# Kernel optimization log

Measured on AMD Instinct MI355X. Metric: run time of the kernel, lower is better.

Reference implementation:

```python
import jax, jax.numpy as jnp
import numpy as np

N, E, B = 200000, 6400000, 128
IN_LOCAL, IN_GLOBAL, HIDDEN, NUM_CLASSES = 16, 8, 32, 2


def setup_inputs() -> dict:
    key = jax.random.key(0)
    ks = jax.random.split(key, 16)
    inp = {
        "x_local": jax.random.normal(ks[0], (N, IN_LOCAL), dtype=jnp.float32),
        "x_global": jax.random.normal(ks[1], (B, IN_GLOBAL), dtype=jnp.float32),
        "batch": jnp.sort(jax.random.randint(ks[2], (N,), 0, B, dtype=jnp.int64)),
        "edge_index": jax.random.randint(ks[3], (2, E), 0, N, dtype=jnp.int64),
        # encoder params
        "W_local": jax.random.normal(ks[4], (IN_LOCAL, HIDDEN), jnp.float32) / np.sqrt(IN_LOCAL),
        "b_local": jnp.zeros((HIDDEN,), jnp.float32),
        "W_global": jax.random.normal(ks[5], (IN_GLOBAL, HIDDEN), jnp.float32) / np.sqrt(IN_GLOBAL),
        "b_global": jnp.zeros((HIDDEN,), jnp.float32),
        "W_mix": jax.random.normal(ks[6], (3 * HIDDEN, HIDDEN), jnp.float32) / np.sqrt(3 * HIDDEN),
        "b_mix": jnp.zeros((HIDDEN,), jnp.float32),
        # GNN layer params
        "W_msg": jax.random.normal(ks[7], (HIDDEN, HIDDEN), jnp.float32) / np.sqrt(HIDDEN),
        "b_msg": jnp.zeros((HIDDEN,), jnp.float32),
        "W_self": jax.random.normal(ks[8], (HIDDEN, HIDDEN), jnp.float32) / np.sqrt(HIDDEN),
        "b_self": jnp.zeros((HIDDEN,), jnp.float32),
        # output head
        "W_out": jax.random.normal(ks[9], (HIDDEN, NUM_CLASSES), jnp.float32) / np.sqrt(HIDDEN),
        "b_out": jnp.zeros((NUM_CLASSES,), jnp.float32),
    }
    return inp


def reference(x_local, x_global, batch, edge_index,
              W_local, b_local, W_global, b_global, W_mix, b_mix,
              W_msg, b_msg, W_self, b_self, W_out, b_out):
    n = x_local.shape[0]
    # --- MixedSelectivityNodeEncoder ---
    h_local = jax.nn.relu(x_local @ W_local + b_local)            # [N,H]
    h_global_graph = jax.nn.relu(x_global @ W_global + b_global)  # [B,H]
    h_global = h_global_graph[batch]                              # gather -> [N,H]
    h_int = h_local * h_global
    h_cat = jnp.concatenate([h_local, h_global, h_int], axis=-1)  # [N,3H]
    h0 = jax.nn.relu(h_cat @ W_mix + b_mix)                       # [N,H]
    # --- GNN layer with self loops, add aggregation ---
    loops = jnp.arange(n, dtype=edge_index.dtype)
    src = jnp.concatenate([edge_index[0], loops])                 # [E+N]
    dst = jnp.concatenate([edge_index[1], loops])                 # [E+N]
    msg = jax.nn.relu(h0[src] @ W_msg + b_msg)                    # [E+N,H]
    aggr = jax.ops.segment_sum(msg, dst, num_segments=n)          # [N,H]
    h = jax.nn.relu(aggr + h0 @ W_self + b_self)                  # [N,H]
    # --- output head ---
    return h @ W_out + b_out                                      # [N,C]
```

## Files before the change

kernel.cpp:

```cpp
#include <hip/hip_runtime.h>

#define N_NODES  200000
#define N_EDGES  6400000
#define NGRAPH   128
#define H        32

#define BNODES   256
#define NBUCK    782
#define P_BLOCKS 256
#define EPB      25000
#define SORT_CAP 8960


typedef unsigned short ushort_t;

__device__ __forceinline__ ushort_t f32_to_bf16_rne(float f) {
    unsigned u = __float_as_uint(f);
    unsigned r = (u + 0x7fffu + ((u >> 16) & 1u)) >> 16;
    return (ushort_t)r;
}
__device__ __forceinline__ float bf16_to_f32(ushort_t h) {
    return __uint_as_float(((unsigned)h) << 16);
}

__global__ __launch_bounds__(256, 1) void k_node_enc(
        const float* __restrict__ xl,
        const int*   __restrict__ batch,
        const float* __restrict__ xg,   const float* __restrict__ Wg,
        const float* __restrict__ bg,
        const float* __restrict__ Wl,   const float* __restrict__ bl,
        const float* __restrict__ Wmix, const float* __restrict__ bmix,
        const float* __restrict__ Wmsg, const float* __restrict__ bmsg,
        const float* __restrict__ Wself,const float* __restrict__ bself,
        ushort_t* __restrict__ mb, float* __restrict__ s) {
    int n0 = blockIdx.x * 256 + threadIdx.x;
    bool valid = (n0 < N_NODES);
    int n = valid ? n0 : (N_NODES - 1);

    float xv[16];
    {
        const float4* p = (const float4*)(xl + (size_t)n * 16);
        float4 a = p[0], b = p[1], c = p[2], d = p[3];
        xv[0]=a.x; xv[1]=a.y; xv[2]=a.z; xv[3]=a.w;
        xv[4]=b.x; xv[5]=b.y; xv[6]=b.z; xv[7]=b.w;
        xv[8]=c.x; xv[9]=c.y; xv[10]=c.z; xv[11]=c.w;
        xv[12]=d.x; xv[13]=d.y; xv[14]=d.z; xv[15]=d.w;
    }
    float gvv[8];
    {
        int gb = batch[n];
        const float4* q = (const float4*)(xg + (size_t)gb * 8);
        float4 a = q[0], b = q[1];
        gvv[0]=a.x; gvv[1]=a.y; gvv[2]=a.z; gvv[3]=a.w;
        gvv[4]=b.x; gvv[5]=b.y; gvv[6]=b.z; gvv[7]=b.w;
    }

    float hl[32], hg[32], hi[32];
#pragma unroll
    for (int t4 = 0; t4 < 8; ++t4) {
        float4 al = ((const float4*)bl)[t4];
        float4 ag = ((const float4*)bg)[t4];
#pragma unroll
        for (int k = 0; k < 16; ++k) {
            float4 w = ((const float4*)(Wl + k * H))[t4];
            al.x = fmaf(xv[k], w.x, al.x); al.y = fmaf(xv[k], w.y, al.y);
            al.z = fmaf(xv[k], w.z, al.z); al.w = fmaf(xv[k], w.w, al.w);
        }
#pragma unroll
        for (int k = 0; k < 8; ++k) {
            float4 w = ((const float4*)(Wg + k * H))[t4];
            ag.x = fmaf(gvv[k], w.x, ag.x); ag.y = fmaf(gvv[k], w.y, ag.y);
            ag.z = fmaf(gvv[k], w.z, ag.z); ag.w = fmaf(gvv[k], w.w, ag.w);
        }
        hl[t4*4+0] = fmaxf(al.x, 0.f); hl[t4*4+1] = fmaxf(al.y, 0.f);
        hl[t4*4+2] = fmaxf(al.z, 0.f); hl[t4*4+3] = fmaxf(al.w, 0.f);
        hg[t4*4+0] = fmaxf(ag.x, 0.f); hg[t4*4+1] = fmaxf(ag.y, 0.f);
        hg[t4*4+2] = fmaxf(ag.z, 0.f); hg[t4*4+3] = fmaxf(ag.w, 0.f);
    }
#pragma unroll
    for (int k = 0; k < 32; ++k) hi[k] = hl[k] * hg[k];

    float h0[32];
#pragma unroll
    for (int t4 = 0; t4 < 8; ++t4) {
        float4 acc = ((const float4*)bmix)[t4];
#pragma unroll
        for (int k = 0; k < 32; ++k) {
            float4 w = ((const float4*)(Wmix + k * H))[t4];
            acc.x = fmaf(hl[k], w.x, acc.x); acc.y = fmaf(hl[k], w.y, acc.y);
            acc.z = fmaf(hl[k], w.z, acc.z); acc.w = fmaf(hl[k], w.w, acc.w);
        }
#pragma unroll
        for (int k = 0; k < 32; ++k) {
            float4 w = ((const float4*)(Wmix + (32 + k) * H))[t4];
            acc.x = fmaf(hg[k], w.x, acc.x); acc.y = fmaf(hg[k], w.y, acc.y);
            acc.z = fmaf(hg[k], w.z, acc.z); acc.w = fmaf(hg[k], w.w, acc.w);
        }
#pragma unroll
        for (int k = 0; k < 32; ++k) {
            float4 w = ((const float4*)(Wmix + (64 + k) * H))[t4];
            acc.x = fmaf(hi[k], w.x, acc.x); acc.y = fmaf(hi[k], w.y, acc.y);
            acc.z = fmaf(hi[k], w.z, acc.z); acc.w = fmaf(hi[k], w.w, acc.w);
        }
        h0[t4*4+0] = fmaxf(acc.x, 0.f); h0[t4*4+1] = fmaxf(acc.y, 0.f);
        h0[t4*4+2] = fmaxf(acc.z, 0.f); h0[t4*4+3] = fmaxf(acc.w, 0.f);
    }

#pragma unroll
    for (int t4 = 0; t4 < 8; ++t4) {
        float4 am = ((const float4*)bmsg)[t4];
        float4 as = ((const float4*)bself)[t4];
#pragma unroll
        for (int k = 0; k < 32; ++k) {
            float4 wm = ((const float4*)(Wmsg + k * H))[t4];
            float4 ws = ((const float4*)(Wself + k * H))[t4];
            am.x = fmaf(h0[k], wm.x, am.x); am.y = fmaf(h0[k], wm.y, am.y);
            am.z = fmaf(h0[k], wm.z, am.z); am.w = fmaf(h0[k], wm.w, am.w);
            as.x = fmaf(h0[k], ws.x, as.x); as.y = fmaf(h0[k], ws.y, as.y);
            as.z = fmaf(h0[k], ws.z, as.z); as.w = fmaf(h0[k], ws.w, as.w);
        }
        if (valid) {
            unsigned d0 = (unsigned)f32_to_bf16_rne(fmaxf(am.x, 0.f))
                        | ((unsigned)f32_to_bf16_rne(fmaxf(am.y, 0.f)) << 16);
            unsigned d1 = (unsigned)f32_to_bf16_rne(fmaxf(am.z, 0.f))
                        | ((unsigned)f32_to_bf16_rne(fmaxf(am.w, 0.f)) << 16);
            ((unsigned*)(mb + (size_t)n * H))[t4*2+0] = d0;
            ((unsigned*)(mb + (size_t)n * H))[t4*2+1] = d1;
            ((float4*)(s + (size_t)n * H))[t4] = as;
        }
    }
}

__global__ __launch_bounds__(1024) void k_ppart(
        const int* __restrict__ ei,
        int* __restrict__ gcur,
        unsigned int* __restrict__ ebuf) {
    __shared__ int cnt[NBUCK];
    __shared__ int basex[NBUCK];
    int t = threadIdx.x, blk = blockIdx.x;
    for (int i = t; i < NBUCK; i += 1024) cnt[i] = 0;
    __syncthreads();

    int e0 = blk * EPB, e1 = e0 + EPB;
    for (int e = e0 + t; e < e1; e += 1024)
        atomicAdd(&cnt[ei[N_EDGES + e] >> 8], 1);
    __syncthreads();

    for (int i = t; i < NBUCK; i += 1024) {
        int c = cnt[i];
        basex[i] = (c > 0) ? atomicAdd(&gcur[i * 32], c) : 0;
    }
    __syncthreads();

    for (int e = e0 + t; e < e1; e += 1024) {
        unsigned src = (unsigned)ei[e];
        int dst = ei[N_EDGES + e];
        int bkt = dst >> 8;
        int pos = atomicAdd(&basex[bkt], 1);
        if (pos < SORT_CAP)
            ebuf[(size_t)bkt * SORT_CAP + pos] = (src << 8) | (unsigned)(dst & 255);
    }
}

__global__ __launch_bounds__(512, 8) void k_bsort_aggr(
        const int* __restrict__ gcur,
        const unsigned int* __restrict__ ebuf,
        const ushort_t* __restrict__ mb, const float* __restrict__ s,
        const float* __restrict__ Wout, const float* __restrict__ bout,
        float* __restrict__ out) {
    __shared__ unsigned sorted[SORT_CAP];
    __shared__ int cnt[BNODES];
    __shared__ int offx[BNODES + 1];
    __shared__ int cur[BNODES];
    __shared__ int wsum[4];
    int tid = threadIdx.x, b = blockIdx.x;

    size_t base = (size_t)b * SORT_CAP;
    int sz = min(gcur[b * 32], SORT_CAP);

    if (tid < BNODES) cnt[tid] = 0;
    __syncthreads();

    for (int j = tid; j < sz; j += 512)
        atomicAdd(&cnt[ebuf[base + j] & 255], 1);
    __syncthreads();

    {
        int lane = tid & 63, w = tid >> 6;
        int v = (tid < BNODES) ? cnt[tid] : 0;
#pragma unroll
        for (int d = 1; d < 64; d <<= 1) {
            int u = __shfl_up(v, d, 64);
            if (lane >= d) v += u;
        }
        if (tid < BNODES && lane == 63) wsum[w] = v;
        __syncthreads();
        if (tid < BNODES) {
            int add = 0;
#pragma unroll
            for (int i = 0; i < 3; ++i) add += (i < w) ? wsum[i] : 0;
            int inc = v + add;
            offx[tid + 1] = inc;
            cur[tid] = inc - cnt[tid];
            if (tid == 0) offx[0] = 0;
        }
        __syncthreads();
    }

    for (int j = tid; j < sz; j += 512) {
        unsigned pk = ebuf[base + j];
        int pos = atomicAdd(&cur[pk & 255], 1);
        sorted[pos] = pk;
    }
    __syncthreads();

    const unsigned* mb32 = (const unsigned*)mb;
    int g = tid >> 4;
    int t = tid & 15;

    for (int q = 0; q < 8; ++q) {
        int loc = (g << 3) + q;
        int n = b * BNODES + loc;
        int rs = offx[loc];
        int re = offx[loc + 1];
        float a0 = 0.f, a1 = 0.f;

        for (int j = rs; j < re; j += 8) {
            unsigned pk[8], u[8];
#pragma unroll
            for (int k = 0; k < 8; ++k)
                pk[k] = sorted[min(j + k, re - 1)];
#pragma unroll
            for (int k = 0; k < 8; ++k)
                u[k] = mb32[(pk[k] >> 8) * 16u + (unsigned)t];
#pragma unroll
            for (int k = 0; k < 8; ++k) {
                bool ok = (j + k < re);
                a0 += ok ? __uint_as_float(u[k] << 16)         : 0.f;
                a1 += ok ? __uint_as_float(u[k] & 0xffff0000u) : 0.f;
            }
        }

        if (n < N_NODES) {
            unsigned u = mb32[(unsigned)n * 16u + (unsigned)t];
            float2 sv = *(const float2*)(s + (size_t)n * H + 2 * t);
            float h0 = fmaxf(a0 + __uint_as_float(u << 16)         + sv.x, 0.f);
            float h1 = fmaxf(a1 + __uint_as_float(u & 0xffff0000u) + sv.y, 0.f);
            float4 w = *(const float4*)(Wout + 4 * t);
            float p0 = h0 * w.x + h1 * w.z;
            float p1 = h0 * w.y + h1 * w.w;
#pragma unroll
            for (int o = 8; o >= 1; o >>= 1) {
                p0 += __shfl_down(p0, o, 16);
                p1 += __shfl_down(p1, o, 16);
            }
            if (t == 0) {
                float2 o2;
                o2.x = p0 + bout[0];
                o2.y = p1 + bout[1];
                *(float2*)(out + (size_t)n * 2) = o2;
            }
        }
    }
}

extern "C" void kernel_launch(void* const* d_in, const int* in_sizes, int n_in,
                              void* d_out, int out_size, void* d_ws, size_t ws_size,
                              hipStream_t stream) {
    const float* xl    = (const float*)d_in[0];
    const float* xg    = (const float*)d_in[1];
    const int*   batch = (const int*)  d_in[2];
    const int*   ei    = (const int*)  d_in[3];
    const float* Wl    = (const float*)d_in[4];
    const float* bl    = (const float*)d_in[5];
    const float* Wg    = (const float*)d_in[6];
    const float* bg    = (const float*)d_in[7];
    const float* Wmix  = (const float*)d_in[8];
    const float* bmix  = (const float*)d_in[9];
    const float* Wmsg  = (const float*)d_in[10];
    const float* bmsg  = (const float*)d_in[11];
    const float* Wself = (const float*)d_in[12];
    const float* bself = (const float*)d_in[13];
    const float* Wout  = (const float*)d_in[14];
    const float* bout  = (const float*)d_in[15];
    float* out = (float*)d_out;

    float*    s    = (float*)d_ws;
    ushort_t* mb   = (ushort_t*)(s + (size_t)N_NODES * H);
    int*      gcur = (int*)(mb + (size_t)N_NODES * H);
    unsigned int* ebuf = (unsigned int*)(gcur + (size_t)NBUCK * 32);

    k_node_enc<<<(N_NODES + 255) / 256, 256, 0, stream>>>(xl, batch, xg, Wg, bg,
                                                          Wl, bl, Wmix, bmix,
                                                          Wmsg, bmsg, Wself, bself,
                                                          mb, s);

    hipMemsetAsync(gcur, 0, (size_t)NBUCK * 32 * sizeof(int), stream);
    k_ppart<<<P_BLOCKS, 1024, 0, stream>>>(ei, gcur, ebuf);
    k_bsort_aggr<<<NBUCK, 512, 0, stream>>>(gcur, ebuf, mb, s, Wout, bout, out);
}
```

Baseline: 367.2 us.

## Merge node encoder and edge partition into one kernel, restructure encoder loops

Fuses the node-encoder kernel and the edge bucket-partition kernel into a single launch, with block index deciding the role, so the compute-bound encoder and the memory-bound partition can run concurrently. The encoder is also reworked to produce h_local/h_global one element at a time and accumulate into the mix output, and the msg and self projections are split into separate loops, all to cut register pressure. The partition blocks now use 256 threads instead of 1024, which lowers per-block parallelism in that phase.

Result: slower. 436.8 us (+18.9%).

```diff
diff --git a/kernel.cpp b/kernel.cpp
--- a/kernel.cpp
+++ b/kernel.cpp
@@ -9,6 +9,7 @@
 #define NBUCK    782
 #define P_BLOCKS 256
 #define EPB      25000
+#define ENC_BLOCKS 782
 #define SORT_CAP 8960
 
 
@@ -23,7 +24,7 @@
     return __uint_as_float(((unsigned)h) << 16);
 }
 
-__global__ __launch_bounds__(256, 1) void k_node_enc(
+__global__ __launch_bounds__(256, 1) void k_enc_part(
         const float* __restrict__ xl,
         const int*   __restrict__ batch,
         const float* __restrict__ xg,   const float* __restrict__ Wg,
@@ -32,8 +33,42 @@
         const float* __restrict__ Wmix, const float* __restrict__ bmix,
         const float* __restrict__ Wmsg, const float* __restrict__ bmsg,
         const float* __restrict__ Wself,const float* __restrict__ bself,
-        ushort_t* __restrict__ mb, float* __restrict__ s) {
-    int n0 = blockIdx.x * 256 + threadIdx.x;
+        ushort_t* __restrict__ mb, float* __restrict__ s,
+        const int* __restrict__ ei,
+        int* __restrict__ gcur,
+        unsigned int* __restrict__ ebuf) {
+    __shared__ int cnt[NBUCK];
+    __shared__ int basex[NBUCK];
+    int tid = threadIdx.x;
+
+    if (blockIdx.x >= ENC_BLOCKS) {
+        int blk = blockIdx.x - ENC_BLOCKS;
+        for (int i = tid; i < NBUCK; i += 256) cnt[i] = 0;
+        __syncthreads();
+
+        int e0 = blk * EPB, e1 = e0 + EPB;
+        for (int e = e0 + tid; e < e1; e += 256)
+            atomicAdd(&cnt[ei[N_EDGES + e] >> 8], 1);
+        __syncthreads();
+
+        for (int i = tid; i < NBUCK; i += 256) {
+            int c = cnt[i];
+            basex[i] = (c > 0) ? atomicAdd(&gcur[i * 32], c) : 0;
+        }
+        __syncthreads();
+
+        for (int e = e0 + tid; e < e1; e += 256) {
+            unsigned src = (unsigned)ei[e];
+            int dst = ei[N_EDGES + e];
+            int bkt = dst >> 8;
+            int pos = atomicAdd(&basex[bkt], 1);
+            if (pos < SORT_CAP)
+                ebuf[(size_t)bkt * SORT_CAP + pos] = (src << 8) | (unsigned)(dst & 255);
+        }
+        return;
+    }
+
+    int n0 = blockIdx.x * 256 + tid;
     bool valid = (n0 < N_NODES);
     int n = valid ? n0 : (N_NODES - 1);
 
@@ -55,69 +90,50 @@
         gvv[4]=b.x; gvv[5]=b.y; gvv[6]=b.z; gvv[7]=b.w;
     }
 
-    float hl[32], hg[32], hi[32];
+    float4 acc4[8];
+#pragma unroll
+    for (int t4 = 0; t4 < 8; ++t4) acc4[t4] = ((const float4*)bmix)[t4];
+
+#pragma unroll
+    for (int k = 0; k < 32; ++k) {
+        float hlk = bl[k];
+#pragma unroll
+        for (int j = 0; j < 16; ++j)
+            hlk = fmaf(xv[j], Wl[j * H + k], hlk);
+        hlk = fmaxf(hlk, 0.f);
+        float hgk = bg[k];
+#pragma unroll
+        for (int j = 0; j < 8; ++j)
+            hgk = fmaf(gvv[j], Wg[j * H + k], hgk);
+        hgk = fmaxf(hgk, 0.f);
+        float hik = hlk * hgk;
+#pragma unroll
+        for (int t4 = 0; t4 < 8; ++t4) {
+            float4 w1 = ((const float4*)(Wmix + k * H))[t4];
+            float4 w2 = ((const float4*)(Wmix + (32 + k) * H))[t4];
+            float4 w3 = ((const float4*)(Wmix + (64 + k) * H))[t4];
+            acc4[t4].x = fmaf(hlk, w1.x, fmaf(hgk, w2.x, fmaf(hik, w3.x, acc4[t4].x)));
+            acc4[t4].y = fmaf(hlk, w1.y, fmaf(hgk, w2.y, fmaf(hik, w3.y, acc4[t4].y)));
+            acc4[t4].z = fmaf(hlk, w1.z, fmaf(hgk, w2.z, fmaf(hik, w3.z, acc4[t4].z)));
+            acc4[t4].w = fmaf(hlk, w1.w, fmaf(hgk, w2.w, fmaf(hik, w3.w, acc4[t4].w)));
+        }
+    }
+
+    float h0[32];
 #pragma unroll
     for (int t4 = 0; t4 < 8; ++t4) {
-        float4 al = ((const float4*)bl)[t4];
-        float4 ag = ((const float4*)bg)[t4];
-#pragma unroll
-        for (int k = 0; k < 16; ++k) {
-            float4 w = ((const float4*)(Wl + k * H))[t4];
-            al.x = fmaf(xv[k], w.x, al.x); al.y = fmaf(xv[k], w.y, al.y);
-            al.z = fmaf(xv[k], w.z, al.z); al.w = fmaf(xv[k], w.w, al.w);
-        }
-#pragma unroll
-        for (int k = 0; k < 8; ++k) {
-            float4 w = ((const float4*)(Wg + k * H))[t4];
-            ag.x = fmaf(gvv[k], w.x, ag.x); ag.y = fmaf(gvv[k], w.y, ag.y);
-            ag.z = fmaf(gvv[k], w.z, ag.z); ag.w = fmaf(gvv[k], w.w, ag.w);
-        }
-        hl[t4*4+0] = fmaxf(al.x, 0.f); hl[t4*4+1] = fmaxf(al.y, 0.f);
-        hl[t4*4+2] = fmaxf(al.z, 0.f); hl[t4*4+3] = fmaxf(al.w, 0.f);
-        hg[t4*4+0] = fmaxf(ag.x, 0.f); hg[t4*4+1] = fmaxf(ag.y, 0.f);
-        hg[t4*4+2] = fmaxf(ag.z, 0.f); hg[t4*4+3] = fmaxf(ag.w, 0.f);
-    }
-#pragma unroll
-    for (int k = 0; k < 32; ++k) hi[k] = hl[k] * hg[k];
-
-    float h0[32];
-#pragma unroll
-    for (int t4 = 0; t4 < 8; ++t4) {
-        float4 acc = ((const float4*)bmix)[t4];
-#pragma unroll
-        for (int k = 0; k < 32; ++k) {
-            float4 w = ((const float4*)(Wmix + k * H))[t4];
-            acc.x = fmaf(hl[k], w.x, acc.x); acc.y = fmaf(hl[k], w.y, acc.y);
-            acc.z = fmaf(hl[k], w.z, acc.z); acc.w = fmaf(hl[k], w.w, acc.w);
-        }
-#pragma unroll
-        for (int k = 0; k < 32; ++k) {
-            float4 w = ((const float4*)(Wmix + (32 + k) * H))[t4];
-            acc.x = fmaf(hg[k], w.x, acc.x); acc.y = fmaf(hg[k], w.y, acc.y);
-            acc.z = fmaf(hg[k], w.z, acc.z); acc.w = fmaf(hg[k], w.w, acc.w);
-        }
-#pragma unroll
-        for (int k = 0; k < 32; ++k) {
-            float4 w = ((const float4*)(Wmix + (64 + k) * H))[t4];
-            acc.x = fmaf(hi[k], w.x, acc.x); acc.y = fmaf(hi[k], w.y, acc.y);
-            acc.z = fmaf(hi[k], w.z, acc.z); acc.w = fmaf(hi[k], w.w, acc.w);
-        }
-        h0[t4*4+0] = fmaxf(acc.x, 0.f); h0[t4*4+1] = fmaxf(acc.y, 0.f);
-        h0[t4*4+2] = fmaxf(acc.z, 0.f); h0[t4*4+3] = fmaxf(acc.w, 0.f);
+        h0[t4*4+0] = fmaxf(acc4[t4].x, 0.f); h0[t4*4+1] = fmaxf(acc4[t4].y, 0.f);
+        h0[t4*4+2] = fmaxf(acc4[t4].z, 0.f); h0[t4*4+3] = fmaxf(acc4[t4].w, 0.f);
     }
 
 #pragma unroll
     for (int t4 = 0; t4 < 8; ++t4) {
         float4 am = ((const float4*)bmsg)[t4];
-        float4 as = ((const float4*)bself)[t4];
 #pragma unroll
         for (int k = 0; k < 32; ++k) {
             float4 wm = ((const float4*)(Wmsg + k * H))[t4];
-            float4 ws = ((const float4*)(Wself + k * H))[t4];
             am.x = fmaf(h0[k], wm.x, am.x); am.y = fmaf(h0[k], wm.y, am.y);
             am.z = fmaf(h0[k], wm.z, am.z); am.w = fmaf(h0[k], wm.w, am.w);
-            as.x = fmaf(h0[k], ws.x, as.x); as.y = fmaf(h0[k], ws.y, as.y);
-            as.z = fmaf(h0[k], ws.z, as.z); as.w = fmaf(h0[k], ws.w, as.w);
         }
         if (valid) {
             unsigned d0 = (unsigned)f32_to_bf16_rne(fmaxf(am.x, 0.f))
@@ -126,39 +142,20 @@
                         | ((unsigned)f32_to_bf16_rne(fmaxf(am.w, 0.f)) << 16);
             ((unsigned*)(mb + (size_t)n * H))[t4*2+0] = d0;
             ((unsigned*)(mb + (size_t)n * H))[t4*2+1] = d1;
+        }
+    }
+
+#pragma unroll
+    for (int t4 = 0; t4 < 8; ++t4) {
+        float4 as = ((const float4*)bself)[t4];
+#pragma unroll
+        for (int k = 0; k < 32; ++k) {
+            float4 ws = ((const float4*)(Wself + k * H))[t4];
+            as.x = fmaf(h0[k], ws.x, as.x); as.y = fmaf(h0[k], ws.y, as.y);
+            as.z = fmaf(h0[k], ws.z, as.z); as.w = fmaf(h0[k], ws.w, as.w);
+        }
+        if (valid)
             ((float4*)(s + (size_t)n * H))[t4] = as;
-        }
-    }
-}
-
-__global__ __launch_bounds__(1024) void k_ppart(
-        const int* __restrict__ ei,
-        int* __restrict__ gcur,
-        unsigned int* __restrict__ ebuf) {
-    __shared__ int cnt[NBUCK];
-    __shared__ int basex[NBUCK];
-    int t = threadIdx.x, blk = blockIdx.x;
-    for (int i = t; i < NBUCK; i += 1024) cnt[i] = 0;
-    __syncthreads();
-
-    int e0 = blk * EPB, e1 = e0 + EPB;
-    for (int e = e0 + t; e < e1; e += 1024)
-        atomicAdd(&cnt[ei[N_EDGES + e] >> 8], 1);
-    __syncthreads();
-
-    for (int i = t; i < NBUCK; i += 1024) {
-        int c = cnt[i];
-        basex[i] = (c > 0) ? atomicAdd(&gcur[i * 32], c) : 0;
-    }
-    __syncthreads();
-
-    for (int e = e0 + t; e < e1; e += 1024) {
-        unsigned src = (unsigned)ei[e];
-        int dst = ei[N_EDGES + e];
-        int bkt = dst >> 8;
-        int pos = atomicAdd(&basex[bkt], 1);
-        if (pos < SORT_CAP)
-            ebuf[(size_t)bkt * SORT_CAP + pos] = (src << 8) | (unsigned)(dst & 255);
     }
 }
 
@@ -290,12 +287,12 @@
     int*      gcur = (int*)(mb + (size_t)N_NODES * H);
     unsigned int* ebuf = (unsigned int*)(gcur + (size_t)NBUCK * 32);
 
-    k_node_enc<<<(N_NODES + 255) / 256, 256, 0, stream>>>(xl, batch, xg, Wg, bg,
-                                                          Wl, bl, Wmix, bmix,
-                                                          Wmsg, bmsg, Wself, bself,
-                                                          mb, s);
-
     hipMemsetAsync(gcur, 0, (size_t)NBUCK * 32 * sizeof(int), stream);
-    k_ppart<<<P_BLOCKS, 1024, 0, stream>>>(ei, gcur, ebuf);
+
+    k_enc_part<<<ENC_BLOCKS + P_BLOCKS, 256, 0, stream>>>(
+        xl, batch, xg, Wg, bg, Wl, bl, Wmix, bmix,
+        Wmsg, bmsg, Wself, bself, mb, s,
+        ei, gcur, ebuf);
+
     k_bsort_aggr<<<NBUCK, 512, 0, stream>>>(gcur, ebuf, mb, s, Wout, bout, out);
 }
```

## Split node encoder across four lanes per node with wave shuffles

Applied to the files above, without the earlier changes.

The node encoder now assigns four threads to each node, with each thread computing eight of the 32 hidden channels. Intermediate activations are exchanged between the four lanes with wave shuffles. This cuts per-thread register pressure, which the old one-node-per-thread version with 96-float arrays had at occupancy 1, and raises parallelism to 3125 blocks. It costs extra shuffle instructions and redundant weight loads per lane. The memset is also moved ahead of the encoder launch.

Result: slower. 456.0 us (+24.2%).

```diff
diff --git a/kernel.cpp b/kernel.cpp
--- a/kernel.cpp
+++ b/kernel.cpp
@@ -19,11 +19,14 @@
     unsigned r = (u + 0x7fffu + ((u >> 16) & 1u)) >> 16;
     return (ushort_t)r;
 }
+__device__ __forceinline__ unsigned pack_bf16x2(float lo, float hi) {
+    return (unsigned)f32_to_bf16_rne(lo) | ((unsigned)f32_to_bf16_rne(hi) << 16);
+}
 __device__ __forceinline__ float bf16_to_f32(ushort_t h) {
     return __uint_as_float(((unsigned)h) << 16);
 }
 
-__global__ __launch_bounds__(256, 1) void k_node_enc(
+__global__ __launch_bounds__(256) void k_enc4(
         const float* __restrict__ xl,
         const int*   __restrict__ batch,
         const float* __restrict__ xg,   const float* __restrict__ Wg,
@@ -33,19 +36,15 @@
         const float* __restrict__ Wmsg, const float* __restrict__ bmsg,
         const float* __restrict__ Wself,const float* __restrict__ bself,
         ushort_t* __restrict__ mb, float* __restrict__ s) {
-    int n0 = blockIdx.x * 256 + threadIdx.x;
-    bool valid = (n0 < N_NODES);
-    int n = valid ? n0 : (N_NODES - 1);
-
-    float xv[16];
-    {
-        const float4* p = (const float4*)(xl + (size_t)n * 16);
-        float4 a = p[0], b = p[1], c = p[2], d = p[3];
-        xv[0]=a.x; xv[1]=a.y; xv[2]=a.z; xv[3]=a.w;
-        xv[4]=b.x; xv[5]=b.y; xv[6]=b.z; xv[7]=b.w;
-        xv[8]=c.x; xv[9]=c.y; xv[10]=c.z; xv[11]=c.w;
-        xv[12]=d.x; xv[13]=d.y; xv[14]=d.z; xv[15]=d.w;
-    }
+    int tid   = threadIdx.x;
+    int r     = tid & 3;
+    int n     = blockIdx.x * 64 + (tid >> 2);
+    int lane  = tid & 63;
+    int gbase = lane & 60;
+    int ch0   = 8 * r;
+
+    float4 xq = ((const float4*)(xl + (size_t)n * 16))[r];
+
     float gvv[8];
     {
         int gb = batch[n];
@@ -55,80 +54,118 @@
         gvv[4]=b.x; gvv[5]=b.y; gvv[6]=b.z; gvv[7]=b.w;
     }
 
-    float hl[32], hg[32], hi[32];
-#pragma unroll
-    for (int t4 = 0; t4 < 8; ++t4) {
-        float4 al = ((const float4*)bl)[t4];
-        float4 ag = ((const float4*)bg)[t4];
-#pragma unroll
-        for (int k = 0; k < 16; ++k) {
-            float4 w = ((const float4*)(Wl + k * H))[t4];
-            al.x = fmaf(xv[k], w.x, al.x); al.y = fmaf(xv[k], w.y, al.y);
-            al.z = fmaf(xv[k], w.z, al.z); al.w = fmaf(xv[k], w.w, al.w);
-        }
-#pragma unroll
-        for (int k = 0; k < 8; ++k) {
-            float4 w = ((const float4*)(Wg + k * H))[t4];
-            ag.x = fmaf(gvv[k], w.x, ag.x); ag.y = fmaf(gvv[k], w.y, ag.y);
-            ag.z = fmaf(gvv[k], w.z, ag.z); ag.w = fmaf(gvv[k], w.w, ag.w);
-        }
-        hl[t4*4+0] = fmaxf(al.x, 0.f); hl[t4*4+1] = fmaxf(al.y, 0.f);
-        hl[t4*4+2] = fmaxf(al.z, 0.f); hl[t4*4+3] = fmaxf(al.w, 0.f);
-        hg[t4*4+0] = fmaxf(ag.x, 0.f); hg[t4*4+1] = fmaxf(ag.y, 0.f);
-        hg[t4*4+2] = fmaxf(ag.z, 0.f); hg[t4*4+3] = fmaxf(ag.w, 0.f);
-    }
-#pragma unroll
-    for (int k = 0; k < 32; ++k) hi[k] = hl[k] * hg[k];
-
-    float h0[32];
-#pragma unroll
-    for (int t4 = 0; t4 < 8; ++t4) {
-        float4 acc = ((const float4*)bmix)[t4];
-#pragma unroll
-        for (int k = 0; k < 32; ++k) {
-            float4 w = ((const float4*)(Wmix + k * H))[t4];
-            acc.x = fmaf(hl[k], w.x, acc.x); acc.y = fmaf(hl[k], w.y, acc.y);
-            acc.z = fmaf(hl[k], w.z, acc.z); acc.w = fmaf(hl[k], w.w, acc.w);
-        }
-#pragma unroll
-        for (int k = 0; k < 32; ++k) {
-            float4 w = ((const float4*)(Wmix + (32 + k) * H))[t4];
-            acc.x = fmaf(hg[k], w.x, acc.x); acc.y = fmaf(hg[k], w.y, acc.y);
-            acc.z = fmaf(hg[k], w.z, acc.z); acc.w = fmaf(hg[k], w.w, acc.w);
-        }
-#pragma unroll
-        for (int k = 0; k < 32; ++k) {
-            float4 w = ((const float4*)(Wmix + (64 + k) * H))[t4];
-            acc.x = fmaf(hi[k], w.x, acc.x); acc.y = fmaf(hi[k], w.y, acc.y);
-            acc.z = fmaf(hi[k], w.z, acc.z); acc.w = fmaf(hi[k], w.w, acc.w);
-        }
-        h0[t4*4+0] = fmaxf(acc.x, 0.f); h0[t4*4+1] = fmaxf(acc.y, 0.f);
-        h0[t4*4+2] = fmaxf(acc.z, 0.f); h0[t4*4+3] = fmaxf(acc.w, 0.f);
-    }
-
-#pragma unroll
-    for (int t4 = 0; t4 < 8; ++t4) {
-        float4 am = ((const float4*)bmsg)[t4];
-        float4 as = ((const float4*)bself)[t4];
-#pragma unroll
-        for (int k = 0; k < 32; ++k) {
-            float4 wm = ((const float4*)(Wmsg + k * H))[t4];
-            float4 ws = ((const float4*)(Wself + k * H))[t4];
-            am.x = fmaf(h0[k], wm.x, am.x); am.y = fmaf(h0[k], wm.y, am.y);
-            am.z = fmaf(h0[k], wm.z, am.z); am.w = fmaf(h0[k], wm.w, am.w);
-            as.x = fmaf(h0[k], ws.x, as.x); as.y = fmaf(h0[k], ws.y, as.y);
-            as.z = fmaf(h0[k], ws.z, as.z); as.w = fmaf(h0[k], ws.w, as.w);
-        }
-        if (valid) {
-            unsigned d0 = (unsigned)f32_to_bf16_rne(fmaxf(am.x, 0.f))
-                        | ((unsigned)f32_to_bf16_rne(fmaxf(am.y, 0.f)) << 16);
-            unsigned d1 = (unsigned)f32_to_bf16_rne(fmaxf(am.z, 0.f))
-                        | ((unsigned)f32_to_bf16_rne(fmaxf(am.w, 0.f)) << 16);
-            ((unsigned*)(mb + (size_t)n * H))[t4*2+0] = d0;
-            ((unsigned*)(mb + (size_t)n * H))[t4*2+1] = d1;
-            ((float4*)(s + (size_t)n * H))[t4] = as;
-        }
-    }
+    float hlr[8];
+    {
+        float4 b0 = *(const float4*)(bl + ch0);
+        float4 b1 = *(const float4*)(bl + ch0 + 4);
+        hlr[0]=b0.x; hlr[1]=b0.y; hlr[2]=b0.z; hlr[3]=b0.w;
+        hlr[4]=b1.x; hlr[5]=b1.y; hlr[6]=b1.z; hlr[7]=b1.w;
+#pragma unroll
+        for (int j = 0; j < 16; ++j) {
+            float xvj = __shfl(((const float*)&xq)[j & 3], gbase | (j >> 2), 64);
+            float4 w0 = *(const float4*)(Wl + j * H + ch0);
+            float4 w1 = *(const float4*)(Wl + j * H + ch0 + 4);
+            hlr[0] = fmaf(xvj, w0.x, hlr[0]); hlr[1] = fmaf(xvj, w0.y, hlr[1]);
+            hlr[2] = fmaf(xvj, w0.z, hlr[2]); hlr[3] = fmaf(xvj, w0.w, hlr[3]);
+            hlr[4] = fmaf(xvj, w1.x, hlr[4]); hlr[5] = fmaf(xvj, w1.y, hlr[5]);
+            hlr[6] = fmaf(xvj, w1.z, hlr[6]); hlr[7] = fmaf(xvj, w1.w, hlr[7]);
+        }
+#pragma unroll
+        for (int i = 0; i < 8; ++i) hlr[i] = fmaxf(hlr[i], 0.f);
+    }
+
+    float hgr[8];
+    {
+        float4 b0 = *(const float4*)(bg + ch0);
+        float4 b1 = *(const float4*)(bg + ch0 + 4);
+        hgr[0]=b0.x; hgr[1]=b0.y; hgr[2]=b0.z; hgr[3]=b0.w;
+        hgr[4]=b1.x; hgr[5]=b1.y; hgr[6]=b1.z; hgr[7]=b1.w;
+#pragma unroll
+        for (int j = 0; j < 8; ++j) {
+            float gj = gvv[j];
+            float4 w0 = *(const float4*)(Wg + j * H + ch0);
+            float4 w1 = *(const float4*)(Wg + j * H + ch0 + 4);
+            hgr[0] = fmaf(gj, w0.x, hgr[0]); hgr[1] = fmaf(gj, w0.y, hgr[1]);
+            hgr[2] = fmaf(gj, w0.z, hgr[2]); hgr[3] = fmaf(gj, w0.w, hgr[3]);
+            hgr[4] = fmaf(gj, w1.x, hgr[4]); hgr[5] = fmaf(gj, w1.y, hgr[5]);
+            hgr[6] = fmaf(gj, w1.z, hgr[6]); hgr[7] = fmaf(gj, w1.w, hgr[7]);
+        }
+#pragma unroll
+        for (int i = 0; i < 8; ++i) hgr[i] = fmaxf(hgr[i], 0.f);
+    }
+
+    float acc[8];
+    {
+        float4 b0 = *(const float4*)(bmix + ch0);
+        float4 b1 = *(const float4*)(bmix + ch0 + 4);
+        acc[0]=b0.x; acc[1]=b0.y; acc[2]=b0.z; acc[3]=b0.w;
+        acc[4]=b1.x; acc[5]=b1.y; acc[6]=b1.z; acc[7]=b1.w;
+    }
+#pragma unroll
+    for (int k = 0; k < 32; ++k) {
+        int owner = gbase | (k >> 3);
+        float hlk = __shfl(hlr[k & 7], owner, 64);
+        float hgk = __shfl(hgr[k & 7], owner, 64);
+        float hik = hlk * hgk;
+        float4 w1a = *(const float4*)(Wmix + k * H + ch0);
+        float4 w1b = *(const float4*)(Wmix + k * H + ch0 + 4);
+        float4 w2a = *(const float4*)(Wmix + (32 + k) * H + ch0);
+        float4 w2b = *(const float4*)(Wmix + (32 + k) * H + ch0 + 4);
+        float4 w3a = *(const float4*)(Wmix + (64 + k) * H + ch0);
+        float4 w3b = *(const float4*)(Wmix + (64 + k) * H + ch0 + 4);
+        acc[0] = fmaf(hlk, w1a.x, fmaf(hgk, w2a.x, fmaf(hik, w3a.x, acc[0])));
+        acc[1] = fmaf(hlk, w1a.y, fmaf(hgk, w2a.y, fmaf(hik, w3a.y, acc[1])));
+        acc[2] = fmaf(hlk, w1a.z, fmaf(hgk, w2a.z, fmaf(hik, w3a.z, acc[2])));
+        acc[3] = fmaf(hlk, w1a.w, fmaf(hgk, w2a.w, fmaf(hik, w3a.w, acc[3])));
+        acc[4] = fmaf(hlk, w1b.x, fmaf(hgk, w2b.x, fmaf(hik, w3b.x, acc[4])));
+        acc[5] = fmaf(hlk, w1b.y, fmaf(hgk, w2b.y, fmaf(hik, w3b.y, acc[5])));
+        acc[6] = fmaf(hlk, w1b.z, fmaf(hgk, w2b.z, fmaf(hik, w3b.z, acc[6])));
+        acc[7] = fmaf(hlk, w1b.w, fmaf(hgk, w2b.w, fmaf(hik, w3b.w, acc[7])));
+    }
+    float h0r[8];
+#pragma unroll
+    for (int i = 0; i < 8; ++i) h0r[i] = fmaxf(acc[i], 0.f);
+
+    float am[8], as[8];
+    {
+        float4 m0 = *(const float4*)(bmsg + ch0);
+        float4 m1 = *(const float4*)(bmsg + ch0 + 4);
+        am[0]=m0.x; am[1]=m0.y; am[2]=m0.z; am[3]=m0.w;
+        am[4]=m1.x; am[5]=m1.y; am[6]=m1.z; am[7]=m1.w;
+        float4 s0 = *(const float4*)(bself + ch0);
+        float4 s1 = *(const float4*)(bself + ch0 + 4);
+        as[0]=s0.x; as[1]=s0.y; as[2]=s0.z; as[3]=s0.w;
+        as[4]=s1.x; as[5]=s1.y; as[6]=s1.z; as[7]=s1.w;
+    }
+#pragma unroll
+    for (int k = 0; k < 32; ++k) {
+        float h0k = __shfl(h0r[k & 7], gbase | (k >> 3), 64);
+        float4 wma = *(const float4*)(Wmsg + k * H + ch0);
+        float4 wmb = *(const float4*)(Wmsg + k * H + ch0 + 4);
+        float4 wsa = *(const float4*)(Wself + k * H + ch0);
+        float4 wsb = *(const float4*)(Wself + k * H + ch0 + 4);
+        am[0] = fmaf(h0k, wma.x, am[0]); am[1] = fmaf(h0k, wma.y, am[1]);
+        am[2] = fmaf(h0k, wma.z, am[2]); am[3] = fmaf(h0k, wma.w, am[3]);
+        am[4] = fmaf(h0k, wmb.x, am[4]); am[5] = fmaf(h0k, wmb.y, am[5]);
+        am[6] = fmaf(h0k, wmb.z, am[6]); am[7] = fmaf(h0k, wmb.w, am[7]);
+        as[0] = fmaf(h0k, wsa.x, as[0]); as[1] = fmaf(h0k, wsa.y, as[1]);
+        as[2] = fmaf(h0k, wsa.z, as[2]); as[3] = fmaf(h0k, wsa.w, as[3]);
+        as[4] = fmaf(h0k, wsb.x, as[4]); as[5] = fmaf(h0k, wsb.y, as[5]);
+        as[6] = fmaf(h0k, wsb.z, as[6]); as[7] = fmaf(h0k, wsb.w, as[7]);
+    }
+
+    uint4 d;
+    d.x = pack_bf16x2(fmaxf(am[0], 0.f), fmaxf(am[1], 0.f));
+    d.y = pack_bf16x2(fmaxf(am[2], 0.f), fmaxf(am[3], 0.f));
+    d.z = pack_bf16x2(fmaxf(am[4], 0.f), fmaxf(am[5], 0.f));
+    d.w = pack_bf16x2(fmaxf(am[6], 0.f), fmaxf(am[7], 0.f));
+    ((uint4*)(mb + (size_t)n * H))[r] = d;
+
+    float4 sv0, sv1;
+    sv0.x = as[0]; sv0.y = as[1]; sv0.z = as[2]; sv0.w = as[3];
+    sv1.x = as[4]; sv1.y = as[5]; sv1.z = as[6]; sv1.w = as[7];
+    ((float4*)(s + (size_t)n * H))[2 * r]     = sv0;
+    ((float4*)(s + (size_t)n * H))[2 * r + 1] = sv1;
 }
 
 __global__ __launch_bounds__(1024) void k_ppart(
@@ -290,12 +327,12 @@
     int*      gcur = (int*)(mb + (size_t)N_NODES * H);
     unsigned int* ebuf = (unsigned int*)(gcur + (size_t)NBUCK * 32);
 
-    k_node_enc<<<(N_NODES + 255) / 256, 256, 0, stream>>>(xl, batch, xg, Wg, bg,
-                                                          Wl, bl, Wmix, bmix,
-                                                          Wmsg, bmsg, Wself, bself,
-                                                          mb, s);
-
     hipMemsetAsync(gcur, 0, (size_t)NBUCK * 32 * sizeof(int), stream);
+
+    k_enc4<<<N_NODES / 64, 256, 0, stream>>>(
+        xl, batch, xg, Wg, bg, Wl, bl, Wmix, bmix,
+        Wmsg, bmsg, Wself, bself, mb, s);
+
     k_ppart<<<P_BLOCKS, 1024, 0, stream>>>(ei, gcur, ebuf);
     k_bsort_aggr<<<NBUCK, 512, 0, stream>>>(gcur, ebuf, mb, s, Wout, bout, out);
 }
```

## Merge edge partition and node encoder into one heterogeneous kernel launch

Applied to the files above, without the earlier changes.

Fuses the edge bucketing kernel and the node encoder into a single launch. The first 256 blocks do the partition, the remaining 782 blocks do the node encoding, so the two independent phases can run concurrently on the GPU and one launch boundary is removed. The partition blocks now use 256 threads instead of 1024, so each block does more serial work and shared-memory atomic parallelism per block drops. The encoder's launch bound of one block per CU may also limit occupancy for the partition blocks.

Measured after the change: 391.8 us. +6.7%, slower.

```diff
diff --git a/kernel.cpp b/kernel.cpp
--- a/kernel.cpp
+++ b/kernel.cpp
@@ -9,6 +9,7 @@
 #define NBUCK    782
 #define P_BLOCKS 256
 #define EPB      25000
+#define ENC_BLOCKS 782
 #define SORT_CAP 8960
 
 
@@ -23,7 +24,10 @@
     return __uint_as_float(((unsigned)h) << 16);
 }
 
-__global__ __launch_bounds__(256, 1) void k_node_enc(
+__global__ __launch_bounds__(256, 1) void k_part_enc(
+        const int*   __restrict__ ei,
+        int*         __restrict__ gcur,
+        unsigned int* __restrict__ ebuf,
         const float* __restrict__ xl,
         const int*   __restrict__ batch,
         const float* __restrict__ xg,   const float* __restrict__ Wg,
@@ -33,7 +37,38 @@
         const float* __restrict__ Wmsg, const float* __restrict__ bmsg,
         const float* __restrict__ Wself,const float* __restrict__ bself,
         ushort_t* __restrict__ mb, float* __restrict__ s) {
-    int n0 = blockIdx.x * 256 + threadIdx.x;
+    __shared__ int cnt[NBUCK];
+    __shared__ int basex[NBUCK];
+    int tid = threadIdx.x;
+
+    if (blockIdx.x < P_BLOCKS) {
+        int blk = blockIdx.x;
+        for (int i = tid; i < NBUCK; i += 256) cnt[i] = 0;
+        __syncthreads();
+
+        int e0 = blk * EPB, e1 = e0 + EPB;
+        for (int e = e0 + tid; e < e1; e += 256)
+            atomicAdd(&cnt[ei[N_EDGES + e] >> 8], 1);
+        __syncthreads();
+
+        for (int i = tid; i < NBUCK; i += 256) {
+            int c = cnt[i];
+            basex[i] = (c > 0) ? atomicAdd(&gcur[i * 32], c) : 0;
+        }
+        __syncthreads();
+
+        for (int e = e0 + tid; e < e1; e += 256) {
+            unsigned src = (unsigned)ei[e];
+            int dst = ei[N_EDGES + e];
+            int bkt = dst >> 8;
+            int pos = atomicAdd(&basex[bkt], 1);
+            if (pos < SORT_CAP)
+                ebuf[(size_t)bkt * SORT_CAP + pos] = (src << 8) | (unsigned)(dst & 255);
+        }
+        return;
+    }
+
+    int n0 = (blockIdx.x - P_BLOCKS) * 256 + tid;
     bool valid = (n0 < N_NODES);
     int n = valid ? n0 : (N_NODES - 1);
 
@@ -128,37 +163,6 @@
             ((unsigned*)(mb + (size_t)n * H))[t4*2+1] = d1;
             ((float4*)(s + (size_t)n * H))[t4] = as;
         }
-    }
-}
-
-__global__ __launch_bounds__(1024) void k_ppart(
-        const int* __restrict__ ei,
-        int* __restrict__ gcur,
-        unsigned int* __restrict__ ebuf) {
-    __shared__ int cnt[NBUCK];
-    __shared__ int basex[NBUCK];
-    int t = threadIdx.x, blk = blockIdx.x;
-    for (int i = t; i < NBUCK; i += 1024) cnt[i] = 0;
-    __syncthreads();
-
-    int e0 = blk * EPB, e1 = e0 + EPB;
-    for (int e = e0 + t; e < e1; e += 1024)
-        atomicAdd(&cnt[ei[N_EDGES + e] >> 8], 1);
-    __syncthreads();
-
-    for (int i = t; i < NBUCK; i += 1024) {
-        int c = cnt[i];
-        basex[i] = (c > 0) ? atomicAdd(&gcur[i * 32], c) : 0;
-    }
-    __syncthreads();
-
-    for (int e = e0 + t; e < e1; e += 1024) {
-        unsigned src = (unsigned)ei[e];
-        int dst = ei[N_EDGES + e];
-        int bkt = dst >> 8;
-        int pos = atomicAdd(&basex[bkt], 1);
-        if (pos < SORT_CAP)
-            ebuf[(size_t)bkt * SORT_CAP + pos] = (src << 8) | (unsigned)(dst & 255);
     }
 }
 
@@ -290,12 +294,12 @@
     int*      gcur = (int*)(mb + (size_t)N_NODES * H);
     unsigned int* ebuf = (unsigned int*)(gcur + (size_t)NBUCK * 32);
 
-    k_node_enc<<<(N_NODES + 255) / 256, 256, 0, stream>>>(xl, batch, xg, Wg, bg,
-                                                          Wl, bl, Wmix, bmix,
-                                                          Wmsg, bmsg, Wself, bself,
-                                                          mb, s);
-
     hipMemsetAsync(gcur, 0, (size_t)NBUCK * 32 * sizeof(int), stream);
-    k_ppart<<<P_BLOCKS, 1024, 0, stream>>>(ei, gcur, ebuf);
+
+    k_part_enc<<<P_BLOCKS + ENC_BLOCKS, 256, 0, stream>>>(
+        ei, gcur, ebuf,
+        xl, batch, xg, Wg, bg, Wl, bl, Wmix, bmix,
+        Wmsg, bmsg, Wself, bself, mb, s);
+
     k_bsort_aggr<<<NBUCK, 512, 0, stream>>>(gcur, ebuf, mb, s, Wout, bout, out);
 }
```
